# Kernel tuning notes

Measured on AMD Instinct MI355X. Metric: run time of the kernel, lower is better.

Reference implementation:

```python
import jax, jax.numpy as jnp
import numpy as np

TRAJ_NUM = 8
EVAL = 30
SGM_T = 2.0
D0 = 0.5
R = 0.3
VOX = 0.2


def setup_inputs() -> dict:
    key = jax.random.key(0)
    ks = jax.random.split(key, 6)
    G, M = 256, 4
    B = G * TRAJ_NUM
    nx, ny, nz = 400, 400, 64
    # quintic boundary matrix at t=0 and t=T; L = A^{-1}
    T = SGM_T
    A = np.array([
        [1, 0, 0, 0, 0, 0],
        [0, 1, 0, 0, 0, 0],
        [0, 0, 2, 0, 0, 0],
        [1, T, T**2, T**3, T**4, T**5],
        [0, 1, 2*T, 3*T**2, 4*T**3, 5*T**4],
        [0, 0, 2, 6*T, 12*T**2, 20*T**3]], dtype=np.float64)
    L = jnp.asarray(np.linalg.inv(A), dtype=jnp.float32)

    def state(k):
        kp, kv, ka = jax.random.split(k, 3)
        # positions inside the 80m x 80m x 12.8m map, away from borders
        p = jax.random.uniform(kp, (B, 3)) * jnp.array([70.0, 70.0, 10.0]) + jnp.array([5.0, 5.0, 1.0])
        v = jax.random.uniform(kv, (B, 3), minval=-1.0, maxval=1.0)
        a = jax.random.uniform(ka, (B, 3), minval=-0.5, maxval=0.5)
        return jnp.stack([p, v, a], axis=-1)  # (B,3,3): rows=axis, cols=[p,v,a]

    Df = state(ks[0])
    Dp = state(ks[1])
    sdf_maps = jax.random.normal(ks[2], (M, nz, ny, nx), dtype=jnp.float32) * 0.5 + 1.0  # (M,D,H,W)
    min_bounds = jnp.zeros((M, 3), jnp.float32)
    sdf_shapes = jnp.tile(jnp.array([[nx, ny, nz]], jnp.float32), (M, 1))  # (nx,ny,nz)
    map_id = jax.random.randint(ks[3], (G,), 0, M)
    return dict(Df=Df, Dp=Dp, L=L, sdf_maps=sdf_maps, min_bounds=min_bounds,
                sdf_shapes=sdf_shapes, map_id=map_id)


def _distance_cost(pos, map_id, sdf_maps, min_bounds, sdf_shapes):
    # pos: (G,N,3) world coords; replicates get_batch_sdf + grid_sample math
    mb = min_bounds[map_id]                           # (G,3)
    shp = sdf_shapes[map_id].astype(jnp.int32)        # (G,3) = (nx,ny,nz)
    mn = jnp.trunc((pos.min(1) - mb) / VOX).astype(jnp.int32)
    mx = jnp.trunc((pos.max(1) - mb) / VOX).astype(jnp.int32)
    max_spans = (mx - mn).max(0)                      # (3,) shared crop span
    c = (mn + mx) // 2
    mn = c - max_spans // 2 - 5
    mx = c + max_spans // 2 + 5
    nmn = jnp.maximum(mn, 0)
    mx = mx + (nmn - mn)
    mn = nmn
    nmx = jnp.minimum(mx, shp)
    mn = mn - (mx - nmx)
    mx = nmx
    shift = jnp.maximum(-jnp.minimum(mn, 0), 0).max(0)  # per-axis over batch
    mn = mn + shift
    local_origin = mn.astype(pos.dtype) * VOX + mb     # (G,3)
    lshape = mx - mn                                   # (G,3) int, crop size

    grid = (pos - local_origin[:, None, :]) / VOX      # local voxel coords (x,y,z)
    gp = 2.0 * grid / (lshape - 1).astype(pos.dtype)[:, None, :] - 1.0
    valid = jnp.all((gp < 0.99) & (gp > -0.99), axis=-1)  # (G,N)

    # trilinear sample, align_corners=True, zeros padding w.r.t. the crop;
    # crop voxel (i,j,k) == full-map voxel (i,j,k)+mn, so gather from the full map
    l0 = jnp.floor(grid).astype(jnp.int32)
    f = grid - l0
    Dm, Hm, Wm = sdf_maps.shape[1:]
    acc = jnp.zeros(pos.shape[:2], pos.dtype)
    for dx in (0, 1):
        for dy in (0, 1):
            for dz in (0, 1):
                il = l0 + jnp.array([dx, dy, dz], jnp.int32)       # (G,N,3) local corner
                inb = jnp.all((il >= 0) & (il < lshape[:, None, :]), axis=-1)
                ig = il + mn[:, None, :]                            # global voxel index
                gx = jnp.clip(ig[..., 0], 0, Wm - 1)
                gy = jnp.clip(ig[..., 1], 0, Hm - 1)
                gz = jnp.clip(ig[..., 2], 0, Dm - 1)
                val = sdf_maps[map_id[:, None], gz, gy, gx]         # (G,N)
                w = ((f[..., 0] if dx else 1 - f[..., 0]) *
                     (f[..., 1] if dy else 1 - f[..., 1]) *
                     (f[..., 2] if dz else 1 - f[..., 2]))
                acc = acc + jnp.where(inb, w * val, 0.0)
    dist = acc
    cost = jnp.exp(-(dist - D0) / R)
    cost = jnp.where(valid, cost, 0.0)
    return cost, dist


def reference(Df, Dp, L, sdf_maps, min_bounds, sdf_shapes, map_id):
    B = Dp.shape[0]
    # coefficients: per axis, coe = L @ [Df_row, Dp_row]
    d = jnp.concatenate([Df, Dp], axis=-1)          # (B,3,6)
    coe = jnp.einsum('jk,bik->bij', L, d)           # (B,3,6)
    dt = SGM_T / EVAL
    t = jnp.linspace(dt, SGM_T, EVAL)               # (30,)
    tp = t[:, None] ** jnp.arange(6)                # (30,6) Vandermonde
    pos = jnp.einsum('nk,bik->bni', tp, coe)        # (B,30,3)
    G = B // TRAJ_NUM
    pos_batch = pos.reshape(G, TRAJ_NUM * EVAL, 3)  # (G,N,3)
    cost, _ = _distance_cost(pos_batch, map_id, sdf_maps, min_bounds, sdf_shapes)
    cost_colli = (cost * dt).reshape(-1, EVAL).sum(-1)  # (B,)
    return cost_colli
```

## Files before the change

### kernel.cpp

```cpp
#include <hip/hip_runtime.h>
#include <hip/hip_bf16.h>
#include <math.h>

#define TRAJ 8
#define EV   30
#define NPT  (TRAJ*EV)
#define GCONST 256
#define MCONST 4
#define NXM  400
#define NYM  400
#define NZM  64

__device__ __forceinline__ float ldf(const void* p, int idx, int isbf) {
    if (isbf) return __bfloat162float(((const __hip_bfloat16*)p)[idx]);
    return ((const float*)p)[idx];
}

__device__ __forceinline__ void resolve_ms(const void*& minb,
                                           const void*& shapes) {
    if (*(const unsigned*)shapes == 0u) {
        const void* t = minb; minb = shapes; shapes = t;
    }
}

__device__ __forceinline__ int detect_bf16(const void* shapes) {
    return *(const unsigned*)shapes != 0x43C80000u;
}

__device__ __forceinline__ void build_coe(const void* Df, const void* Dp,
                                          const void* L, int g, int isbf,
                                          float* sL, float* scoe, int t) {
#pragma clang fp contract(off)
    if (t < 36) sL[t] = ldf(L, t, isbf);
    __syncthreads();
    if (t < 144) {
        int traj = t / 18, rem = t % 18, i = rem / 6, j = rem % 6;
        int b = g * TRAJ + traj;
        float dv[6];
#pragma unroll
        for (int k = 0; k < 3; ++k) {
            dv[k]     = ldf(Df, b * 9 + i * 3 + k, isbf);
            dv[3 + k] = ldf(Dp, b * 9 + i * 3 + k, isbf);
        }
        float s = 0.f;
#pragma unroll
        for (int k = 0; k < 6; ++k) s = s + sL[j * 6 + k] * dv[k];
        scoe[(traj * 3 + i) * 6 + j] = s;
    }
    __syncthreads();
}

__device__ __forceinline__ void eval_pos(const float* scoe, int traj, int e,
                                         double* p) {
    const double dt   = 2.0 / 30.0;
    const double step = (2.0 - dt) / 29.0;
    double tn = (e == EV - 1) ? 2.0 : dt + (double)e * step;
    double tk = 1.0;
    p[0] = p[1] = p[2] = 0.0;
#pragma unroll
    for (int k = 0; k < 6; ++k) {
        p[0] += tk * (double)scoe[(traj * 3 + 0) * 6 + k];
        p[1] += tk * (double)scoe[(traj * 3 + 1) * 6 + k];
        p[2] += tk * (double)scoe[(traj * 3 + 2) * 6 + k];
        tk *= tn;
    }
}

__global__ __launch_bounds__(256) void k_minmax(
    const void* Df, const void* Dp, const void* L, const void* minb_in,
    const void* shapes_in, const int* map_id, int* groupA) {
    __shared__ float  sL[36];
    __shared__ float  scoe[144];
    __shared__ double smin[3][256];
    __shared__ double smax[3][256];
    const void* minb = minb_in; const void* shapes = shapes_in;
    resolve_ms(minb, shapes);
    int g = blockIdx.x, t = threadIdx.x;
    int isbf = detect_bf16(shapes);
    build_coe(Df, Dp, L, g, isbf, sL, scoe, t);

    double p[3] = {0.0, 0.0, 0.0};
    if (t < NPT) eval_pos(scoe, t / EV, t % EV, p);
#pragma unroll
    for (int i = 0; i < 3; ++i) {
        smin[i][t] = (t < NPT) ? p[i] : 1e300;
        smax[i][t] = (t < NPT) ? p[i] : -1e300;
    }
    for (int off = 128; off; off >>= 1) {
        __syncthreads();
        if (t < off)
#pragma unroll
            for (int i = 0; i < 3; ++i) {
                smin[i][t] = fmin(smin[i][t], smin[i][t + off]);
                smax[i][t] = fmax(smax[i][t], smax[i][t + off]);
            }
    }
    __syncthreads();
    if (t == 0) {
        int mid = min(max(map_id[g], 0), MCONST - 1);
#pragma unroll
        for (int i = 0; i < 3; ++i) {
            double mb = (double)ldf(minb, mid * 3 + i, isbf);
            groupA[g * 8 + i]     = (int)trunc((smin[i][0] - mb) / 0.2);
            groupA[g * 8 + 4 + i] = (int)trunc((smax[i][0] - mb) / 0.2);
        }
    }
}

__global__ __launch_bounds__(256) void k_window(
    const int* groupA, int* groupB, const int* map_id, const void* minb_in,
    const void* shapes_in) {
    __shared__ int sred[3][256];
    const void* minb = minb_in; const void* shapes = shapes_in;
    resolve_ms(minb, shapes);
    int t = threadIdx.x;
    int isbf = detect_bf16(shapes);
    const int G = GCONST;

    int spmax[3] = {0, 0, 0};
    for (int g = t; g < G; g += 256)
#pragma unroll
        for (int i = 0; i < 3; ++i) {
            int sp = groupA[g * 8 + 4 + i] - groupA[g * 8 + i];
            if (sp > spmax[i]) spmax[i] = sp;
        }
#pragma unroll
    for (int i = 0; i < 3; ++i) sred[i][t] = spmax[i];
    for (int off = 128; off; off >>= 1) {
        __syncthreads();
        if (t < off)
#pragma unroll
            for (int i = 0; i < 3; ++i)
                sred[i][t] = max(sred[i][t], sred[i][t + off]);
    }
    __syncthreads();
    int span[3] = {sred[0][0], sred[1][0], sred[2][0]};
    __syncthreads();

    int negmax[3] = {0, 0, 0};
    for (int g = t; g < G; g += 256) {
        int mid = min(max(map_id[g], 0), MCONST - 1);
#pragma unroll
        for (int i = 0; i < 3; ++i) {
            int mn0 = groupA[g * 8 + i], mx0 = groupA[g * 8 + 4 + i];
            int c   = (mn0 + mx0) >> 1;
            int h   = span[i] >> 1;
            int mn1 = c - h - 5, mx1 = c + h + 5;
            int nmn = mn1 > 0 ? mn1 : 0;
            int mx2 = mx1 + (nmn - mn1);
            int shp = (int)ldf(shapes, mid * 3 + i, isbf);
            int nmx = mx2 < shp ? mx2 : shp;
            int mn3 = nmn - (mx2 - nmx);
            groupB[g * 8 + i]     = mn3;
            groupB[g * 8 + 4 + i] = nmx;
            int neg = mn3 < 0 ? -mn3 : 0;
            if (neg > negmax[i]) negmax[i] = neg;
        }
    }
#pragma unroll
    for (int i = 0; i < 3; ++i) sred[i][t] = negmax[i];
    for (int off = 128; off; off >>= 1) {
        __syncthreads();
        if (t < off)
#pragma unroll
            for (int i = 0; i < 3; ++i)
                sred[i][t] = max(sred[i][t], sred[i][t + off]);
    }
    __syncthreads();
    int shift[3] = {sred[0][0], sred[1][0], sred[2][0]};

    for (int g = t; g < G; g += 256)
#pragma unroll
        for (int i = 0; i < 3; ++i) {
            int mnf = groupB[g * 8 + i] + shift[i];
            int lsh = groupB[g * 8 + 4 + i] - mnf;
            groupB[g * 8 + i]     = mnf;
            groupB[g * 8 + 4 + i] = lsh;
        }
}

__global__ __launch_bounds__(256) void k_sample(
    const void* Df, const void* Dp, const void* L, const void* minb_in,
    const void* shapes_in, const int* map_id, const void* sdf,
    const int* groupB, float* out) {
    __shared__ float  sL[36];
    __shared__ float  scoe[144];
    __shared__ double scost[NPT];
    const void* minb = minb_in; const void* shapes = shapes_in;
    resolve_ms(minb, shapes);
    int g = blockIdx.x, t = threadIdx.x;
    int isbf = detect_bf16(shapes);
    build_coe(Df, Dp, L, g, isbf, sL, scoe, t);

    int mid = min(max(map_id[g], 0), MCONST - 1);
    int mnf[3], lsh[3];
#pragma unroll
    for (int i = 0; i < 3; ++i) {
        mnf[i] = groupB[g * 8 + i];
        lsh[i] = groupB[g * 8 + 4 + i];
    }

    if (t < NPT) {
        double p[3];
        eval_pos(scoe, t / EV, t % EV, p);
        double f[3];
        int    l0[3];
        bool   valid = true;
#pragma unroll
        for (int i = 0; i < 3; ++i) {
            double mb = (double)ldf(minb, mid * 3 + i, isbf);
            double gr = (p[i] - ((double)mnf[i] * 0.2 + mb)) / 0.2;
            double gp = 2.0 * gr / (double)(lsh[i] - 1) - 1.0;
            valid = valid && (gp < 0.99) && (gp > -0.99);
            double fl = floor(gr);
            l0[i] = (int)fl;
            f[i]  = gr - fl;
        }
        int    mbase = mid * (NZM * NYM * NXM);
        double acc   = 0.0;
#pragma unroll
        for (int dx = 0; dx < 2; ++dx) {
            int  ilx = l0[0] + dx;
            bool bx  = ilx >= 0 && ilx < lsh[0];
            int  gx  = min(max(ilx + mnf[0], 0), NXM - 1);
            double wx = dx ? f[0] : 1.0 - f[0];
#pragma unroll
            for (int dy = 0; dy < 2; ++dy) {
                int  ily = l0[1] + dy;
                bool by  = ily >= 0 && ily < lsh[1];
                int  gy  = min(max(ily + mnf[1], 0), NYM - 1);
                double wy = dy ? f[1] : 1.0 - f[1];
#pragma unroll
                for (int dz = 0; dz < 2; ++dz) {
                    int  ilz = l0[2] + dz;
                    bool bz  = ilz >= 0 && ilz < lsh[2];
                    int  gz  = min(max(ilz + mnf[2], 0), NZM - 1);
                    double wz = dz ? f[2] : 1.0 - f[2];
                    if (bx && by && bz) {
                        int idx = mbase + (gz * NYM + gy) * NXM + gx;
                        acc += wx * wy * wz * (double)ldf(sdf, idx, isbf);
                    }
                }
            }
        }
        double cost = valid ? exp(-(acc - 0.5) / 0.3) : 0.0;
        scost[t] = cost * (2.0 / 30.0);
    }
    __syncthreads();
    if (t < TRAJ) {
        double s = 0.0;
#pragma unroll
        for (int e = 0; e < EV; ++e) s += scost[t * EV + e];
        out[g * TRAJ + t] = (float)s;
    }
}

extern "C" void kernel_launch(void* const* d_in, const int* in_sizes, int n_in,
                              void* d_out, int out_size, void* d_ws,
                              size_t ws_size, hipStream_t stream) {
    int order[16];
    int n = n_in < 16 ? n_in : 16;
    for (int i = 0; i < n; ++i) order[i] = i;
    for (int i = 1; i < n; ++i) {
        int oi = order[i], j = i - 1;
        while (j >= 0 && in_sizes[order[j]] < in_sizes[oi]) {
            order[j + 1] = order[j]; --j;
        }
        order[j + 1] = oi;
    }
    const void* sdf    = d_in[order[0]];
    const void* Df     = d_in[order[1]];
    const void* Dp     = d_in[order[2]];
    const int*  map_id = (const int*)d_in[order[3]];
    const void* L      = d_in[order[4]];
    const void* minb   = d_in[order[5]];
    const void* shapes = d_in[order[6 < n ? 6 : 5]];

    int* groupA = (int*)d_ws;
    int* groupB = groupA + GCONST * 8;

    k_minmax<<<GCONST, 256, 0, stream>>>(Df, Dp, L, minb, shapes, map_id,
                                         groupA);
    k_window<<<1, 256, 0, stream>>>(groupA, groupB, map_id, minb, shapes);
    k_sample<<<GCONST, 256, 0, stream>>>(Df, Dp, L, minb, shapes, map_id, sdf,
                                         groupB, (float*)d_out);
    (void)out_size; (void)ws_size;
}
```

Measured before the change: 222.6 us.

## Fuse window computation into sample kernel and batch trilinear gathers

```diff
diff --git a/kernel.cpp b/kernel.cpp
--- a/kernel.cpp
+++ b/kernel.cpp
@@ -107,25 +107,27 @@
     }
 }
 
-__global__ __launch_bounds__(256) void k_window(
-    const int* groupA, int* groupB, const int* map_id, const void* minb_in,
-    const void* shapes_in) {
-    __shared__ int sred[3][256];
+__global__ __launch_bounds__(256) void k_sample(
+    const void* Df, const void* Dp, const void* L, const void* minb_in,
+    const void* shapes_in, const int* map_id, const void* sdf,
+    const int* groupA, float* out) {
+    __shared__ float  sL[36];
+    __shared__ float  scoe[144];
+    __shared__ double scost[NPT];
+    __shared__ int    sWin[GCONST][6];
+    __shared__ int    sred[3][256];
     const void* minb = minb_in; const void* shapes = shapes_in;
     resolve_ms(minb, shapes);
-    int t = threadIdx.x;
+    int g = blockIdx.x, t = threadIdx.x;
     int isbf = detect_bf16(shapes);
-    const int G = GCONST;
-
-    int spmax[3] = {0, 0, 0};
-    for (int g = t; g < G; g += 256)
-#pragma unroll
-        for (int i = 0; i < 3; ++i) {
-            int sp = groupA[g * 8 + 4 + i] - groupA[g * 8 + i];
-            if (sp > spmax[i]) spmax[i] = sp;
-        }
-#pragma unroll
-    for (int i = 0; i < 3; ++i) sred[i][t] = spmax[i];
+
+    int mn0[3], mx0[3];
+#pragma unroll
+    for (int i = 0; i < 3; ++i) {
+        mn0[i] = groupA[t * 8 + i];
+        mx0[i] = groupA[t * 8 + 4 + i];
+        sred[i][t] = mx0[i] - mn0[i];
+    }
     for (int off = 128; off; off >>= 1) {
         __syncthreads();
         if (t < off)
@@ -137,28 +139,23 @@
     int span[3] = {sred[0][0], sred[1][0], sred[2][0]};
     __syncthreads();
 
-    int negmax[3] = {0, 0, 0};
-    for (int g = t; g < G; g += 256) {
-        int mid = min(max(map_id[g], 0), MCONST - 1);
+    {
+        int mid_t = min(max(map_id[t], 0), MCONST - 1);
 #pragma unroll
         for (int i = 0; i < 3; ++i) {
-            int mn0 = groupA[g * 8 + i], mx0 = groupA[g * 8 + 4 + i];
-            int c   = (mn0 + mx0) >> 1;
+            int c   = (mn0[i] + mx0[i]) >> 1;
             int h   = span[i] >> 1;
             int mn1 = c - h - 5, mx1 = c + h + 5;
             int nmn = mn1 > 0 ? mn1 : 0;
             int mx2 = mx1 + (nmn - mn1);
-            int shp = (int)ldf(shapes, mid * 3 + i, isbf);
+            int shp = (int)ldf(shapes, mid_t * 3 + i, isbf);
             int nmx = mx2 < shp ? mx2 : shp;
             int mn3 = nmn - (mx2 - nmx);
-            groupB[g * 8 + i]     = mn3;
-            groupB[g * 8 + 4 + i] = nmx;
-            int neg = mn3 < 0 ? -mn3 : 0;
-            if (neg > negmax[i]) negmax[i] = neg;
-        }
-    }
-#pragma unroll
-    for (int i = 0; i < 3; ++i) sred[i][t] = negmax[i];
+            sWin[t][i]     = mn3;
+            sWin[t][3 + i] = nmx;
+            sred[i][t]     = mn3 < 0 ? -mn3 : 0;
+        }
+    }
     for (int off = 128; off; off >>= 1) {
         __syncthreads();
         if (t < off)
@@ -167,39 +164,18 @@
                 sred[i][t] = max(sred[i][t], sred[i][t + off]);
     }
     __syncthreads();
-    int shift[3] = {sred[0][0], sred[1][0], sred[2][0]};
-
-    for (int g = t; g < G; g += 256)
-#pragma unroll
-        for (int i = 0; i < 3; ++i) {
-            int mnf = groupB[g * 8 + i] + shift[i];
-            int lsh = groupB[g * 8 + 4 + i] - mnf;
-            groupB[g * 8 + i]     = mnf;
-            groupB[g * 8 + 4 + i] = lsh;
-        }
-}
-
-__global__ __launch_bounds__(256) void k_sample(
-    const void* Df, const void* Dp, const void* L, const void* minb_in,
-    const void* shapes_in, const int* map_id, const void* sdf,
-    const int* groupB, float* out) {
-    __shared__ float  sL[36];
-    __shared__ float  scoe[144];
-    __shared__ double scost[NPT];
-    const void* minb = minb_in; const void* shapes = shapes_in;
-    resolve_ms(minb, shapes);
-    int g = blockIdx.x, t = threadIdx.x;
-    int isbf = detect_bf16(shapes);
+    int mnf[3], lsh[3];
+#pragma unroll
+    for (int i = 0; i < 3; ++i) {
+        int m  = sWin[g][i] + sred[i][0];
+        mnf[i] = m;
+        lsh[i] = sWin[g][3 + i] - m;
+    }
+    __syncthreads();
+
     build_coe(Df, Dp, L, g, isbf, sL, scoe, t);
 
     int mid = min(max(map_id[g], 0), MCONST - 1);
-    int mnf[3], lsh[3];
-#pragma unroll
-    for (int i = 0; i < 3; ++i) {
-        mnf[i] = groupB[g * 8 + i];
-        lsh[i] = groupB[g * 8 + 4 + i];
-    }
-
     if (t < NPT) {
         double p[3];
         eval_pos(scoe, t / EV, t % EV, p);
@@ -216,33 +192,31 @@
             l0[i] = (int)fl;
             f[i]  = gr - fl;
         }
-        int    mbase = mid * (NZM * NYM * NXM);
-        double acc   = 0.0;
-#pragma unroll
-        for (int dx = 0; dx < 2; ++dx) {
-            int  ilx = l0[0] + dx;
-            bool bx  = ilx >= 0 && ilx < lsh[0];
-            int  gx  = min(max(ilx + mnf[0], 0), NXM - 1);
-            double wx = dx ? f[0] : 1.0 - f[0];
-#pragma unroll
-            for (int dy = 0; dy < 2; ++dy) {
-                int  ily = l0[1] + dy;
-                bool by  = ily >= 0 && ily < lsh[1];
-                int  gy  = min(max(ily + mnf[1], 0), NYM - 1);
-                double wy = dy ? f[1] : 1.0 - f[1];
-#pragma unroll
-                for (int dz = 0; dz < 2; ++dz) {
-                    int  ilz = l0[2] + dz;
-                    bool bz  = ilz >= 0 && ilz < lsh[2];
-                    int  gz  = min(max(ilz + mnf[2], 0), NZM - 1);
-                    double wz = dz ? f[2] : 1.0 - f[2];
-                    if (bx && by && bz) {
-                        int idx = mbase + (gz * NYM + gy) * NXM + gx;
-                        acc += wx * wy * wz * (double)ldf(sdf, idx, isbf);
-                    }
-                }
-            }
-        }
+        const int mbase = mid * (NZM * NYM * NXM);
+        int  idx8[8];
+        bool inb8[8];
+        double w8[8];
+#pragma unroll
+        for (int c = 0; c < 8; ++c) {
+            int dx = c & 1, dy = (c >> 1) & 1, dz = (c >> 2) & 1;
+            int ilx = l0[0] + dx, ily = l0[1] + dy, ilz = l0[2] + dz;
+            inb8[c] = (ilx >= 0 && ilx < lsh[0]) && (ily >= 0 && ily < lsh[1])
+                   && (ilz >= 0 && ilz < lsh[2]);
+            int gx = min(max(ilx + mnf[0], 0), NXM - 1);
+            int gy = min(max(ily + mnf[1], 0), NYM - 1);
+            int gz = min(max(ilz + mnf[2], 0), NZM - 1);
+            idx8[c] = mbase + (gz * NYM + gy) * NXM + gx;
+            w8[c] = (dx ? f[0] : 1.0 - f[0]) * (dy ? f[1] : 1.0 - f[1])
+                  * (dz ? f[2] : 1.0 - f[2]);
+        }
+        float v8[8];
+#pragma unroll
+        for (int c = 0; c < 8; ++c) v8[c] = ldf(sdf, idx8[c], isbf);
+        double acc = 0.0;
+#pragma unroll
+        for (int c = 0; c < 8; ++c)
+            if (inb8[c]) acc += w8[c] * (double)v8[c];
+
         double cost = valid ? exp(-(acc - 0.5) / 0.3) : 0.0;
         scost[t] = cost * (2.0 / 30.0);
     }
@@ -277,12 +251,10 @@
     const void* shapes = d_in[order[6 < n ? 6 : 5]];
 
     int* groupA = (int*)d_ws;
-    int* groupB = groupA + GCONST * 8;
 
     k_minmax<<<GCONST, 256, 0, stream>>>(Df, Dp, L, minb, shapes, map_id,
                                          groupA);
-    k_window<<<1, 256, 0, stream>>>(groupA, groupB, map_id, minb, shapes);
     k_sample<<<GCONST, 256, 0, stream>>>(Df, Dp, L, minb, shapes, map_id, sdf,
-                                         groupB, (float*)d_out);
+                                         groupA, (float*)d_out);
     (void)out_size; (void)ws_size;
 }
```

After: 218.8 us. No clear change (-1.7%).
